# Performance work log

Hardware: AMD Instinct MI355X
Metric: run time of the kernel (lower is better)

Reference implementation:

```python
import jax, jax.numpy as jnp
import numpy as np

L, H, C = 2, 2, 128            # conv layers, heads, out_channels
N, E, B = 10000, 100000, 64    # nodes, edges, graphs
F_NODE, F_EDGE, FC = 92, 50, 512
HC, C3 = H * C, 3 * C


def _ln(x, g, b, eps=1e-5):
    m = x.mean(-1, keepdims=True)
    v = jnp.var(x, axis=-1, keepdims=True)
    return (x - m) * jax.lax.rsqrt(v + eps) * g + b


def setup_inputs() -> dict:
    key = jax.random.key(0)
    ks = jax.random.split(key, 20)
    r = lambda i, shape, s=0.05: jax.random.normal(ks[i], shape, jnp.float32) * s
    d = {}
    d["x"] = jax.random.normal(ks[0], (N, F_NODE), jnp.float32)
    d["edge_attr"] = jax.random.normal(ks[1], (E, F_EDGE), jnp.float32)
    d["pge"] = jax.random.normal(ks[2], (B, 32), jnp.float32)
    d["cse"] = jax.random.normal(ks[3], (B, 7), jnp.float32)
    d["edge_index"] = jax.random.randint(ks[4], (2, E), 0, N, jnp.int32)
    d["batch"] = jnp.sort(jax.random.randint(ks[5], (N,), 0, B, jnp.int32))
    d["atom_W"] = r(6, (F_NODE, C)); d["atom_b"] = jnp.zeros(C)
    d["edge_W"] = r(7, (F_EDGE, C)); d["edge_b"] = jnp.zeros(C)
    d["Wq"] = r(8, (L, C, HC)); d["bq"] = jnp.zeros((L, HC))
    d["Wk"] = r(9, (L, C, HC)); d["bk"] = jnp.zeros((L, HC))
    d["Wv"] = r(10, (L, C, HC)); d["bv"] = jnp.zeros((L, HC))
    d["We"] = r(11, (L, C, HC))
    d["Wmu"] = r(12, (L, C3, C3)); d["bmu"] = jnp.zeros((L, C3))
    d["Wm"] = r(13, (L, C3, C)); d["bm"] = jnp.zeros((L, C))
    d["ln_m_g"] = jnp.ones((L, C)); d["ln_m_b"] = jnp.zeros((L, C))
    d["ln_a_g"] = jnp.ones((L, C3)); d["ln_a_b"] = jnp.zeros((L, C3))
    d["Wc"] = r(14, (L, HC, C)); d["bc"] = jnp.zeros((L, C))
    d["bn_g"] = jnp.ones((L, C)); d["bn_b"] = jnp.zeros((L, C))
    d["Wskip"] = r(15, (L, C, C)); d["bskip"] = jnp.zeros((L, C))
    d["fc_W"] = r(16, (C + 32 + 7, FC)); d["fc_b"] = jnp.zeros(FC)
    d["out_W"] = r(17, (FC, 1)); d["out_b"] = jnp.zeros(1)
    return d


def reference(x, edge_attr, pge, cse, edge_index, batch, atom_W, atom_b,
              edge_W, edge_b, Wq, bq, Wk, bk, Wv, bv, We, Wmu, bmu, Wm, bm,
              ln_m_g, ln_m_b, ln_a_g, ln_a_b, Wc, bc, bn_g, bn_b, Wskip,
              bskip, fc_W, fc_b, out_W, out_b):
    src, dst = edge_index[0], edge_index[1]  # j = source, i = target
    nf = x @ atom_W + atom_b                 # [N, C]
    ef = edge_attr @ edge_W + edge_b         # [E, C]
    scale = 1.0 / np.sqrt(C3).astype(np.float32)
    for i in range(L):
        q = (nf @ Wq[i] + bq[i]).reshape(N, H, C)
        k = (nf @ Wk[i] + bk[i]).reshape(N, H, C)
        v = (nf @ Wv[i] + bv[i]).reshape(N, H, C)
        ea = (ef @ We[i]).reshape(E, H, C)
        qi = q[dst]
        qcat = jnp.concatenate([qi, qi, qi], -1)                 # [E,H,3C]
        kcat = jnp.concatenate([k[dst], k[src], ea], -1)         # [E,H,3C]
        alpha = qcat * kcat * scale
        gate = jax.nn.sigmoid(_ln(alpha, ln_a_g[i], ln_a_b[i]))
        m = jnp.concatenate([v[dst], v[src], ea], -1)            # [E,H,3C]
        m = (jnp.einsum('ehf,fg->ehg', m, Wmu[i]) + bmu[i]) * gate
        m = jnp.einsum('ehf,fc->ehc', m, Wm[i]) + bm[i]          # [E,H,C]
        m = _ln(m, ln_m_g[i], ln_m_b[i])
        agg = jax.ops.segment_sum(m, dst, num_segments=N)        # scatter-add
        o = agg.reshape(N, HC) @ Wc[i] + bc[i]                   # lin_concate
        mu = o.mean(0); var = jnp.var(o, axis=0)                 # BN (batch stats)
        o = (o - mu) * jax.lax.rsqrt(var + 1e-5) * bn_g[i] + bn_b[i]
        o = jax.nn.silu(o)
        nf = o + nf @ Wskip[i] + bskip[i]                        # root skip
    sums = jax.ops.segment_sum(nf, batch, num_segments=B)
    cnt = jax.ops.segment_sum(jnp.ones((N, 1), nf.dtype), batch, num_segments=B)
    pooled = sums / jnp.maximum(cnt, 1.0)                        # global_mean_pool
    feats = jnp.concatenate([pooled, pge, cse], 1)               # [B, C+39]
    h = jax.nn.silu(feats @ fc_W + fc_b)
    return h @ out_W + out_b                                     # [B, 1]
```

## Files before the change

### kernel.cpp

```cpp
#include <hip/hip_runtime.h>
#include <math.h>

#define N_NODES 10000
#define N_EDGES 100000
#define N_GRAPH 64
#define CDIM 128
#define HCDIM 256
#define C3DIM 384

typedef unsigned short u16;
typedef __attribute__((ext_vector_type(8))) short bf16x8;
typedef __attribute__((ext_vector_type(4))) float f32x4;

__device__ __forceinline__ u16 f2bf(float f) {
  union { float f; unsigned int u; } x; x.f = f;
  unsigned int u = x.u + 0x7fffu + ((x.u >> 16) & 1u);
  return (u16)(u >> 16);
}
__device__ __forceinline__ float bf2f(u16 h) {
  union { unsigned int u; float f; } x; x.u = ((unsigned int)h) << 16;
  return x.f;
}

template<int ACT>
__global__ __launch_bounds__(256) void gemm_kernel(
    const float* __restrict__ A, const float* __restrict__ W,
    const float* __restrict__ bias, float* __restrict__ Y,
    u16* __restrict__ Yb, int M, int K, int N) {
  __shared__ float As[16][68];
  __shared__ float Bs[16][65];
  const int tid = threadIdx.x;
  const int bm = blockIdx.y * 64, bn = blockIdx.x * 64;
  const int tx = tid & 15, ty = tid >> 4;
  float acc[4][4] = {};
  for (int k0 = 0; k0 < K; k0 += 16) {
#pragma unroll
    for (int i = 0; i < 4; ++i) {
      int l = tid + i * 256;
      int kk = l & 15, m = l >> 4;
      int gm = bm + m, gk = k0 + kk;
      As[kk][m] = (gm < M && gk < K) ? A[(size_t)gm * K + gk] : 0.f;
    }
#pragma unroll
    for (int i = 0; i < 4; ++i) {
      int l = tid + i * 256;
      int n = l & 63, kk = l >> 6;
      int gk = k0 + kk, gn = bn + n;
      Bs[kk][n] = (gk < K && gn < N) ? W[(size_t)gk * N + gn] : 0.f;
    }
    __syncthreads();
#pragma unroll
    for (int kk = 0; kk < 16; ++kk) {
      float a[4], b[4];
#pragma unroll
      for (int i = 0; i < 4; ++i) a[i] = As[kk][ty * 4 + i];
#pragma unroll
      for (int j = 0; j < 4; ++j) b[j] = Bs[kk][tx * 4 + j];
#pragma unroll
      for (int i = 0; i < 4; ++i)
#pragma unroll
        for (int j = 0; j < 4; ++j) acc[i][j] += a[i] * b[j];
    }
    __syncthreads();
  }
#pragma unroll
  for (int i = 0; i < 4; ++i) {
    int gm = bm + ty * 4 + i;
    if (gm >= M) continue;
#pragma unroll
    for (int j = 0; j < 4; ++j) {
      int gn = bn + tx * 4 + j;
      if (gn >= N) continue;
      float val = acc[i][j] + (bias ? bias[gn] : 0.f);
      if (ACT == 1) val = val / (1.f + expf(-val));
      if (Y)  Y[(size_t)gm * N + gn] = val;
      if (Yb) Yb[(size_t)gm * N + gn] = f2bf(val);
    }
  }
}

template<int OUT_BF16>
__global__ __launch_bounds__(256) void mfma_gemm_kernel(
    const u16* __restrict__ Ab, const u16* __restrict__ WT,
    const float* __restrict__ bias, void* __restrict__ Y,
    int M, int K, int N) {
  const int tid = threadIdx.x;
  const int w = tid >> 6, l = tid & 63;
  const int lq = l >> 4, ln = l & 15;
  const int bm = blockIdx.y * 128, bn = blockIdx.x * 64;
  int ra = bm + w * 32 + ln;      if (ra > M - 1) ra = M - 1;
  int rb = bm + w * 32 + 16 + ln; if (rb > M - 1) rb = M - 1;
  f32x4 acc[2][4];
#pragma unroll
  for (int g = 0; g < 2; ++g)
#pragma unroll
    for (int nt = 0; nt < 4; ++nt) acc[g][nt] = {0.f, 0.f, 0.f, 0.f};
  for (int k0 = 0; k0 < K; k0 += 32) {
    bf16x8 a0 = *(const bf16x8*)&Ab[(size_t)ra * K + k0 + lq * 8];
    bf16x8 a1 = *(const bf16x8*)&Ab[(size_t)rb * K + k0 + lq * 8];
#pragma unroll
    for (int nt = 0; nt < 4; ++nt) {
      bf16x8 b = *(const bf16x8*)&WT[(size_t)(bn + nt * 16 + ln) * K + k0 + lq * 8];
      acc[0][nt] = __builtin_amdgcn_mfma_f32_16x16x32_bf16(a0, b, acc[0][nt], 0, 0, 0);
      acc[1][nt] = __builtin_amdgcn_mfma_f32_16x16x32_bf16(a1, b, acc[1][nt], 0, 0, 0);
    }
  }
#pragma unroll
  for (int g = 0; g < 2; ++g) {
    int rowbase = bm + w * 32 + g * 16 + lq * 4;
#pragma unroll
    for (int nt = 0; nt < 4; ++nt) {
      int gn = bn + nt * 16 + ln;
      float bv = bias ? bias[gn] : 0.f;
#pragma unroll
      for (int r = 0; r < 4; ++r) {
        int gm = rowbase + r;
        if (gm < M) {
          float val = acc[g][nt][r] + bv;
          if (OUT_BF16) ((u16*)Y)[(size_t)gm * N + gn] = f2bf(val);
          else          ((float*)Y)[(size_t)gm * N + gn] = val;
        }
      }
    }
  }
}

__global__ __launch_bounds__(256) void compose_kernel(
    const float* __restrict__ Wv, const float* __restrict__ We,
    const float* __restrict__ Wmu, float* __restrict__ WP12,
    float* __restrict__ WPe) {
  const int z = blockIdx.z;
  const float* Ap; const float* Bp; float* Cp; int ldc;
  if (z < 4) {
    int part = z >> 1, h = z & 1;
    Ap = Wv + h * 128; Bp = Wmu + part * 128 * 384;
    Cp = WP12 + part * 768 + h * 384; ldc = 1536;
  } else {
    int h = z - 4;
    Ap = We + h * 128; Bp = Wmu + 256 * 384;
    Cp = WPe + h * 384; ldc = 768;
  }
  __shared__ float As[16][68];
  __shared__ float Bs[16][65];
  const int tid = threadIdx.x;
  const int bm = blockIdx.y * 64, bn = blockIdx.x * 64;
  const int tx = tid & 15, ty = tid >> 4;
  float acc[4][4] = {};
  for (int k0 = 0; k0 < 128; k0 += 16) {
#pragma unroll
    for (int i = 0; i < 4; ++i) {
      int l = tid + i * 256;
      int kk = l & 15, m = l >> 4;
      As[kk][m] = Ap[(size_t)(bm + m) * 256 + k0 + kk];
    }
#pragma unroll
    for (int i = 0; i < 4; ++i) {
      int l = tid + i * 256;
      int n = l & 63, kk = l >> 6;
      Bs[kk][n] = Bp[(size_t)(k0 + kk) * 384 + bn + n];
    }
    __syncthreads();
#pragma unroll
    for (int kk = 0; kk < 16; ++kk) {
      float a[4], b[4];
#pragma unroll
      for (int i = 0; i < 4; ++i) a[i] = As[kk][ty * 4 + i];
#pragma unroll
      for (int j = 0; j < 4; ++j) b[j] = Bs[kk][tx * 4 + j];
#pragma unroll
      for (int i = 0; i < 4; ++i)
#pragma unroll
        for (int j = 0; j < 4; ++j) acc[i][j] += a[i] * b[j];
    }
    __syncthreads();
  }
#pragma unroll
  for (int i = 0; i < 4; ++i)
#pragma unroll
    for (int j = 0; j < 4; ++j)
      Cp[(size_t)(bm + ty * 4 + i) * ldc + bn + tx * 4 + j] = acc[i][j];
}

__global__ void pack_all_kernel(
    const float* __restrict__ Wq, const float* __restrict__ Wk,
    const float* __restrict__ Wc, const float* __restrict__ Wsk,
    const float* __restrict__ Wm_l, const float* __restrict__ bmu,
    const float* __restrict__ bv_l, const float* __restrict__ Wmu,
    const float* __restrict__ bq_l, const float* __restrict__ bk_l,
    u16* __restrict__ WallT, u16* __restrict__ WcTw, u16* __restrict__ WskT,
    u16* __restrict__ WmTb, float* __restrict__ cbv, float* __restrict__ ball) {
  int z = blockIdx.y;
  int idx = blockIdx.x * 256 + threadIdx.x;
  if (z == 0) {
    if (idx < 32768) { int col = idx >> 7, kk = idx & 127;
      WallT[(size_t)col * 128 + kk] = f2bf(Wq[(size_t)kk * 256 + col]); }
  } else if (z == 1) {
    if (idx < 32768) { int col = idx >> 7, kk = idx & 127;
      WallT[(size_t)(256 + col) * 128 + kk] = f2bf(Wk[(size_t)kk * 256 + col]); }
  } else if (z == 2) {
    if (idx < 32768) { int col = idx >> 8, kk = idx & 255;
      WcTw[(size_t)col * 256 + kk] = f2bf(Wc[(size_t)kk * 128 + col]); }
  } else if (z == 3) {
    if (idx < 16384) { int col = idx >> 7, kk = idx & 127;
      WskT[(size_t)col * 128 + kk] = f2bf(Wsk[(size_t)kk * 128 + col]); }
  } else if (z == 4) {
    if (idx < 49152) { int col = idx / 384, kk = idx - col * 384;
      WmTb[idx] = f2bf(Wm_l[(size_t)kk * 128 + col]); }
  } else if (z == 5) {
    if (idx < 768) {
      int h2 = idx / 384, g = idx - h2 * 384;
      float s = bmu[g];
      for (int d = 0; d < 128; ++d)
        s += bv_l[h2 * 128 + d] * (Wmu[(size_t)d * 384 + g] + Wmu[(size_t)(128 + d) * 384 + g]);
      cbv[idx] = s;
    }
  } else {
    if (idx < 2048) {
      float v = 0.f;
      if (idx < 256) v = bq_l[idx];
      else if (idx < 512) v = bk_l[idx - 256];
      ball[idx] = v;
    }
  }
}

__global__ void packcomb_kernel(const float* __restrict__ We_l,
                                const float* __restrict__ WPe,
                                const float* __restrict__ WP12,
                                u16* __restrict__ WcT, u16* __restrict__ WallT) {
  int z = blockIdx.y;
  int idx = blockIdx.x * 256 + threadIdx.x;
  if (z == 0) {
    if (idx < 131072) { int col = idx >> 7, kk = idx & 127;
      float v = (col < 256) ? We_l[(size_t)kk * 256 + col]
                            : WPe[(size_t)kk * 768 + (col - 256)];
      WcT[idx] = f2bf(v); }
  } else {
    if (idx < 196608) { int col = idx >> 7, kk = idx & 127;
      WallT[(size_t)(512 + col) * 128 + kk] = f2bf(WP12[(size_t)kk * 1536 + col]); }
  }
}

__global__ void pack_bf16_kernel(const float* __restrict__ A, u16* __restrict__ B, int n) {
  int idx = blockIdx.x * blockDim.x + threadIdx.x;
  if (idx < n) B[idx] = f2bf(A[idx]);
}

__global__ __launch_bounds__(256, 3) void edge_kernel(
    const u16* __restrict__ qkp, const u16* __restrict__ efb,
    const int* __restrict__ ei, const u16* __restrict__ WcT,
    const float* __restrict__ cbv,
    const float* __restrict__ lag, const float* __restrict__ lab,
    const u16* __restrict__ WmT, const float* __restrict__ bm_l,
    const float* __restrict__ lmg, const float* __restrict__ lmb,
    float* __restrict__ agg, int E) {
  __shared__ __align__(16) u16 C1[16 * 1032];
  __shared__ __align__(16) u16 A2p[12 * 512];
  __shared__ int did16[16];
  float* C2 = (float*)A2p;
  const int tid = threadIdx.x;
  const int e0 = blockIdx.x * 16;
  const int w = tid >> 6, l = tid & 63;
  const int lq = l >> 4, ln = l & 15;
  const float scale = 0.051031036307982884f;

  if (tid < 16) did16[tid] = ei[E + e0 + tid];

  const int r = tid >> 4, lx = tid & 15;
  const int hA = r >> 3, eA = r & 7;

  bf16x8 qv[2], kdv[2], ksv[2], pdv[2][3], psv[2][3];
#pragma unroll
  for (int s = 0; s < 2; ++s) {
    int edge = e0 + s * 8 + eA;
    int dstn = ei[E + edge], srcn = ei[edge];
    const u16* db = qkp + (size_t)dstn * 2048;
    const u16* sb = qkp + (size_t)srcn * 2048;
    qv[s]  = *(const bf16x8*)&db[hA * 128 + lx * 8];
    kdv[s] = *(const bf16x8*)&db[256 + hA * 128 + lx * 8];
    ksv[s] = *(const bf16x8*)&sb[256 + hA * 128 + lx * 8];
#pragma unroll
    for (int p = 0; p < 3; ++p) {
      pdv[s][p] = *(const bf16x8*)&db[512 + hA * 384 + p * 128 + lx * 8];
      psv[s][p] = *(const bf16x8*)&sb[512 + 768 + hA * 384 + p * 128 + lx * 8];
    }
  }

  {
    bf16x8 afr[4];
    const u16* ab = efb + (size_t)(e0 + ln) * 128 + lq * 8;
#pragma unroll
    for (int ks = 0; ks < 4; ++ks) afr[ks] = *(const bf16x8*)(ab + ks * 32);
    for (int nt = 0; nt < 16; ++nt) {
      int g = w * 16 + nt;
      const u16* bb = WcT + (size_t)(g * 16 + ln) * 128 + lq * 8;
      f32x4 acc = {0.f, 0.f, 0.f, 0.f};
#pragma unroll
      for (int ks = 0; ks < 4; ++ks)
        acc = __builtin_amdgcn_mfma_f32_16x16x32_bf16(
            afr[ks], *(const bf16x8*)(bb + ks * 32), acc, 0, 0, 0);
      int col = g * 16 + ln;
#pragma unroll
      for (int rr = 0; rr < 4; ++rr) C1[(lq * 4 + rr) * 1032 + col] = f2bf(acc[rr]);
    }
  }
  __syncthreads();

  for (int s = 0; s < 2; ++s) {
    {
      bf16x8 sea = *(const bf16x8*)&C1[(s * 8 + eA) * 1032 + hA * 128 + lx * 8];
      float a0[8], a1[8], a2[8];
      float sacc = 0.f, s2acc = 0.f;
#pragma unroll
      for (int j = 0; j < 8; ++j) {
        float qf = bf2f((u16)qv[s][j]);
        float x0 = qf * bf2f((u16)kdv[s][j]) * scale;
        float x1 = qf * bf2f((u16)ksv[s][j]) * scale;
        float x2 = qf * bf2f((u16)sea[j]) * scale;
        a0[j] = x0; a1[j] = x1; a2[j] = x2;
        sacc += x0 + x1 + x2;
        s2acc += x0 * x0 + x1 * x1 + x2 * x2;
      }
#pragma unroll
      for (int mm = 1; mm < 16; mm <<= 1) {
        sacc += __shfl_xor(sacc, mm); s2acc += __shfl_xor(s2acc, mm);
      }
      float mean = sacc * (1.f / C3DIM);
      float rstd = rsqrtf(s2acc * (1.f / C3DIM) - mean * mean + 1e-5f);
#pragma unroll
      for (int p = 0; p < 3; ++p) {
        const float* lg = lag + p * 128 + lx * 8;
        const float* lb = lab + p * 128 + lx * 8;
        f32x4 g0 = *(const f32x4*)lg, g1 = *(const f32x4*)(lg + 4);
        f32x4 b0 = *(const f32x4*)lb, b1 = *(const f32x4*)(lb + 4);
        f32x4 c0 = *(const f32x4*)&cbv[hA * 384 + p * 128 + lx * 8];
        f32x4 c1 = *(const f32x4*)&cbv[hA * 384 + p * 128 + lx * 8 + 4];
        bf16x8 pe = *(const bf16x8*)&C1[(s * 8 + eA) * 1032 + 256 + hA * 384 + p * 128 + lx * 8];
        bf16x8 outv;
#pragma unroll
        for (int j = 0; j < 8; ++j) {
          float av = p == 0 ? a0[j] : (p == 1 ? a1[j] : a2[j]);
          float gg = j < 4 ? g0[j] : g1[j - 4];
          float bb2 = j < 4 ? b0[j] : b1[j - 4];
          float cbj = j < 4 ? c0[j] : c1[j - 4];
          float z = (av - mean) * rstd * gg + bb2;
          float gate = 1.f / (1.f + expf(-z));
          float t = (bf2f((u16)pe[j]) + bf2f((u16)pdv[s][p][j]) +
                     bf2f((u16)psv[s][p][j]) + cbj) * gate;
          outv[j] = (short)f2bf(t);
        }
        int ks = p * 4 + (lx >> 2), qq = lx & 3;
        int slot = (((r ^ (qq << 2)) + ks) & 15) | (qq << 4);
        *(bf16x8*)&A2p[ks * 512 + slot * 8] = outv;
      }
    }
    __syncthreads();

    {
      bf16x8 af2[12];
#pragma unroll
      for (int ks = 0; ks < 12; ++ks) {
        int slot = (((ln ^ (lq << 2)) + ks) & 15) | (lq << 4);
        af2[ks] = *(const bf16x8*)&A2p[ks * 512 + slot * 8];
      }
      __syncthreads();
#pragma unroll
      for (int nt = 0; nt < 2; ++nt) {
        int g = w * 2 + nt;
        const u16* bb = WmT + (size_t)(g * 16 + ln) * 384 + lq * 8;
        f32x4 acc = {0.f, 0.f, 0.f, 0.f};
#pragma unroll
        for (int ks = 0; ks < 12; ++ks)
          acc = __builtin_amdgcn_mfma_f32_16x16x32_bf16(
              af2[ks], *(const bf16x8*)(bb + ks * 32), acc, 0, 0, 0);
        int col = g * 16 + ln;
        float bcol = bm_l[col];
#pragma unroll
        for (int rr = 0; rr < 4; ++rr) C2[(lq * 4 + rr) * 132 + col] = acc[rr] + bcol;
      }
    }
    __syncthreads();

    {
      for (int rw = w; rw < 16; rw += 4) {
        float v0 = C2[rw * 132 + l], v1 = C2[rw * 132 + l + 64];
        float sa = v0 + v1, s2a = v0 * v0 + v1 * v1;
#pragma unroll
        for (int off2 = 32; off2 > 0; off2 >>= 1) {
          sa += __shfl_down(sa, off2); s2a += __shfl_down(s2a, off2);
        }
        sa = __shfl(sa, 0); s2a = __shfl(s2a, 0);
        float mean = sa * (1.f / CDIM);
        float rstd = rsqrtf(s2a * (1.f / CDIM) - mean * mean + 1e-5f);
        int h = rw >> 3, e = rw & 7;
        int dstn = did16[s * 8 + e];
        float o0 = (v0 - mean) * rstd * lmg[l] + lmb[l];
        float o1 = (v1 - mean) * rstd * lmg[l + 64] + lmb[l + 64];
        atomicAdd(&agg[(size_t)dstn * HCDIM + h * CDIM + l], o0);
        atomicAdd(&agg[(size_t)dstn * HCDIM + h * CDIM + l + 64], o1);
      }
    }
    __syncthreads();
  }
}

__global__ __launch_bounds__(256) void bn_stats_kernel(
    const float* __restrict__ o, float* __restrict__ mu, float* __restrict__ rstd) {
  int c = blockIdx.x, tid = threadIdx.x;
  float s = 0.f, s2 = 0.f;
  for (int r = tid; r < N_NODES; r += 256) {
    float x = o[(size_t)r * CDIM + c];
    s += x; s2 += x * x;
  }
  __shared__ float red[8];
#pragma unroll
  for (int off = 32; off > 0; off >>= 1) {
    s += __shfl_down(s, off); s2 += __shfl_down(s2, off);
  }
  if ((tid & 63) == 0) { red[tid >> 6] = s; red[4 + (tid >> 6)] = s2; }
  __syncthreads();
  if (tid == 0) {
    float ts = red[0] + red[1] + red[2] + red[3];
    float t2 = red[4] + red[5] + red[6] + red[7];
    float m = ts * (1.f / N_NODES);
    float var = t2 * (1.f / N_NODES) - m * m;
    mu[c] = m;
    rstd[c] = rsqrtf(var + 1e-5f);
  }
}

__global__ void bn_silu_skip_kernel(
    const float* __restrict__ o, const float* __restrict__ skip,
    const float* __restrict__ mu, const float* __restrict__ rstd,
    const float* __restrict__ g, const float* __restrict__ b,
    float* __restrict__ nf, u16* __restrict__ nfb) {
  int idx = blockIdx.x * blockDim.x + threadIdx.x;
  if (idx >= N_NODES * CDIM) return;
  int c = idx & (CDIM - 1);
  float x = (o[idx] - mu[c]) * rstd[c] * g[c] + b[c];
  float sig = 1.f / (1.f + expf(-x));
  float val = x * sig + skip[idx];
  nf[idx] = val;
  nfb[idx] = f2bf(val);
}

__global__ void pool_kernel(const float* __restrict__ nf, const int* __restrict__ batch,
                            float* __restrict__ psum, float* __restrict__ cnt) {
  int idx = blockIdx.x * blockDim.x + threadIdx.x;
  if (idx >= N_NODES * CDIM) return;
  int n = idx >> 7, c = idx & 127;
  int b = batch[n];
  atomicAdd(&psum[b * CDIM + c], nf[idx]);
  if (c == 0) atomicAdd(&cnt[b], 1.f);
}

__global__ void feats_kernel(const float* __restrict__ psum, const float* __restrict__ cnt,
                             const float* __restrict__ pge, const float* __restrict__ cse,
                             float* __restrict__ feats) {
  int idx = blockIdx.x * blockDim.x + threadIdx.x;
  if (idx >= N_GRAPH * 167) return;
  int b = idx / 167, j = idx - b * 167;
  float val;
  if (j < 128)      val = psum[b * CDIM + j] / fmaxf(cnt[b], 1.f);
  else if (j < 160) val = pge[b * 32 + (j - 128)];
  else              val = cse[b * 7 + (j - 160)];
  feats[idx] = val;
}

__global__ __launch_bounds__(256) void out_kernel(
    const float* __restrict__ h, const float* __restrict__ ow,
    const float* __restrict__ ob, float* __restrict__ out) {
  int b = blockIdx.x, tid = threadIdx.x;
  float s = h[b * 512 + tid] * ow[tid] + h[b * 512 + tid + 256] * ow[tid + 256];
  __shared__ float red[4];
#pragma unroll
  for (int off = 32; off > 0; off >>= 1) s += __shfl_down(s, off);
  if ((tid & 63) == 0) red[tid >> 6] = s;
  __syncthreads();
  if (tid == 0) out[b] = red[0] + red[1] + red[2] + red[3] + ob[0];
}

extern "C" void kernel_launch(void* const* d_in, const int* in_sizes, int n_in,
                              void* d_out, int out_size, void* d_ws, size_t ws_size,
                              hipStream_t stream) {
  const float* x         = (const float*)d_in[0];
  const float* edge_attr = (const float*)d_in[1];
  const float* pge       = (const float*)d_in[2];
  const float* cse       = (const float*)d_in[3];
  const int*   ei        = (const int*)d_in[4];
  const int*   batch     = (const int*)d_in[5];
  const float* atom_W    = (const float*)d_in[6];
  const float* atom_b    = (const float*)d_in[7];
  const float* edge_W    = (const float*)d_in[8];
  const float* edge_b    = (const float*)d_in[9];
  const float* Wq        = (const float*)d_in[10];
  const float* bq        = (const float*)d_in[11];
  const float* Wk        = (const float*)d_in[12];
  const float* bk        = (const float*)d_in[13];
  const float* Wv        = (const float*)d_in[14];
  const float* bv        = (const float*)d_in[15];
  const float* We        = (const float*)d_in[16];
  const float* Wmu       = (const float*)d_in[17];
  const float* bmu       = (const float*)d_in[18];
  const float* Wm        = (const float*)d_in[19];
  const float* bm        = (const float*)d_in[20];
  const float* ln_m_g    = (const float*)d_in[21];
  const float* ln_m_b    = (const float*)d_in[22];
  const float* ln_a_g    = (const float*)d_in[23];
  const float* ln_a_b    = (const float*)d_in[24];
  const float* Wc        = (const float*)d_in[25];
  const float* bc        = (const float*)d_in[26];
  const float* bn_g      = (const float*)d_in[27];
  const float* bn_b      = (const float*)d_in[28];
  const float* Wskip     = (const float*)d_in[29];
  const float* bskip     = (const float*)d_in[30];
  const float* fc_W      = (const float*)d_in[31];
  const float* fc_b      = (const float*)d_in[32];
  const float* out_W     = (const float*)d_in[33];
  const float* out_b     = (const float*)d_in[34];

  float* ws = (float*)d_ws;
  size_t off = 0;
  float* nf    = ws + off; off += (size_t)N_NODES * CDIM;
  float* agg   = ws + off; off += (size_t)N_NODES * HCDIM;
  float* o     = ws + off; off += (size_t)N_NODES * CDIM;
  float* skip  = ws + off; off += (size_t)N_NODES * CDIM;
  float* WP12  = ws + off; off += (size_t)128 * 1536;
  float* WPe   = ws + off; off += (size_t)128 * 768;
  float* cbv   = ws + off; off += 768;
  float* ball  = ws + off; off += 2048;
  float* mu    = ws + off; off += CDIM;
  float* rstd  = ws + off; off += CDIM;
  float* psum  = ws + off; off += (size_t)N_GRAPH * CDIM;
  float* cnt   = ws + off; off += N_GRAPH;
  float* feats = ws + off; off += (size_t)N_GRAPH * 167;
  float* h     = ws + off; off += (size_t)N_GRAPH * 512;
  u16* efb   = (u16*)(ws + off); off += (size_t)N_EDGES * 64;
  u16* WcT   = (u16*)(ws + off); off += 65536;
  u16* WmTb  = (u16*)(ws + off); off += 24576;
  u16* nfb   = (u16*)(ws + off); off += (size_t)N_NODES * 64;
  u16* aggb  = (u16*)(ws + off); off += (size_t)N_NODES * 128;
  u16* qkp   = (u16*)(ws + off); off += (size_t)N_NODES * 1024;
  u16* WallT = (u16*)(ws + off); off += 131072;
  u16* WcTw  = (u16*)(ws + off); off += 16384;
  u16* WskT  = (u16*)(ws + off); off += 8192;

  auto mgemm = [&](const u16* Ab, const u16* WT, const float* bias, void* Y,
                   int M, int K, int Nn, int out_bf16) {
    dim3 grid(Nn / 64, (M + 127) / 128);
    if (out_bf16) mfma_gemm_kernel<1><<<grid, 256, 0, stream>>>(Ab, WT, bias, Y, M, K, Nn);
    else          mfma_gemm_kernel<0><<<grid, 256, 0, stream>>>(Ab, WT, bias, Y, M, K, Nn);
  };

  gemm_kernel<0><<<dim3(2, 157), 256, 0, stream>>>(x, atom_W, atom_b, nf, nfb,
                                                   N_NODES, 92, CDIM);
  gemm_kernel<0><<<dim3(2, 1563), 256, 0, stream>>>(edge_attr, edge_W, edge_b,
                                                    nullptr, efb, N_EDGES, 50, CDIM);

  for (int i = 0; i < 2; ++i) {
    const float* Wv_i  = Wv + (size_t)i * CDIM * HCDIM;
    const float* We_i  = We + (size_t)i * CDIM * HCDIM;
    const float* Wmu_i = Wmu + (size_t)i * C3DIM * C3DIM;
    compose_kernel<<<dim3(6, 2, 6), 256, 0, stream>>>(Wv_i, We_i, Wmu_i, WP12, WPe);
    pack_all_kernel<<<dim3(192, 7), 256, 0, stream>>>(
        Wq + (size_t)i * CDIM * HCDIM, Wk + (size_t)i * CDIM * HCDIM,
        Wc + (size_t)i * HCDIM * CDIM, Wskip + (size_t)i * CDIM * CDIM,
        Wm + (size_t)i * C3DIM * CDIM, bmu + i * C3DIM, bv + i * HCDIM, Wmu_i,
        bq + i * HCDIM, bk + i * HCDIM,
        WallT, WcTw, WskT, WmTb, cbv, ball);
    packcomb_kernel<<<dim3(768, 2), 256, 0, stream>>>(We_i, WPe, WP12, WcT, WallT);

    mgemm(nfb, WallT, ball, qkp, N_NODES, CDIM, 2048, 1);

    hipMemsetAsync(agg, 0, (size_t)N_NODES * HCDIM * sizeof(float), stream);
    edge_kernel<<<dim3(N_EDGES / 16), dim3(256), 0, stream>>>(
        qkp, efb, ei, WcT, cbv,
        ln_a_g + i * C3DIM, ln_a_b + i * C3DIM,
        WmTb, bm + i * CDIM,
        ln_m_g + i * CDIM, ln_m_b + i * CDIM, agg, N_EDGES);

    pack_bf16_kernel<<<dim3((N_NODES * 256 + 255) / 256), dim3(256), 0, stream>>>(
        agg, aggb, N_NODES * 256);
    mgemm(aggb, WcTw, bc + i * CDIM, o, N_NODES, HCDIM, CDIM, 0);
    bn_stats_kernel<<<dim3(CDIM), dim3(256), 0, stream>>>(o, mu, rstd);
    mgemm(nfb, WskT, bskip + i * CDIM, skip, N_NODES, CDIM, CDIM, 0);
    bn_silu_skip_kernel<<<dim3((N_NODES * CDIM + 255) / 256), dim3(256), 0, stream>>>(
        o, skip, mu, rstd, bn_g + i * CDIM, bn_b + i * CDIM, nf, nfb);
  }

  hipMemsetAsync(psum, 0, (size_t)(N_GRAPH * CDIM + N_GRAPH) * sizeof(float), stream);
  pool_kernel<<<dim3((N_NODES * CDIM + 255) / 256), dim3(256), 0, stream>>>(nf, batch, psum, cnt);
  feats_kernel<<<dim3((N_GRAPH * 167 + 255) / 256), dim3(256), 0, stream>>>(psum, cnt, pge, cse, feats);
  gemm_kernel<1><<<dim3(8, 1), 256, 0, stream>>>(feats, fc_W, fc_b, h, nullptr,
                                                 N_GRAPH, 167, 512);
  out_kernel<<<dim3(N_GRAPH), 256, 0, stream>>>(h, out_W, out_b, (float*)d_out);
}
```

Measured before the change: 1.360 ms.

## Sort edges by destination, pre-reduce scatter atomics, fuse BN stats and memsets

Builds a destination-sorted edge permutation with histogram, scan and scatter kernels, so the edge kernel processes edges grouped by target node. Each warp can then accumulate consecutive same-destination contributions in registers before issuing atomics. It also moves the input embeddings to bf16 MFMA GEMMs with padded packing, folds BatchNorm column statistics into the output GEMM via atomics, and folds the agg and pool memsets into existing kernels. This trades extra setup kernels and a permuted gather on edge features for fewer global atomics and launches. The fused statistics compute variance as E[x^2]-m^2 on float atomics, which is less exact than the old two-pass reduction.

```diff
diff --git a/kernel.cpp b/kernel.cpp
--- a/kernel.cpp
+++ b/kernel.cpp
@@ -26,7 +26,7 @@
 __global__ __launch_bounds__(256) void gemm_kernel(
     const float* __restrict__ A, const float* __restrict__ W,
     const float* __restrict__ bias, float* __restrict__ Y,
-    u16* __restrict__ Yb, int M, int K, int N) {
+    int M, int K, int N) {
   __shared__ float As[16][68];
   __shared__ float Bs[16][65];
   const int tid = threadIdx.x;
@@ -73,16 +73,16 @@
       if (gn >= N) continue;
       float val = acc[i][j] + (bias ? bias[gn] : 0.f);
       if (ACT == 1) val = val / (1.f + expf(-val));
-      if (Y)  Y[(size_t)gm * N + gn] = val;
-      if (Yb) Yb[(size_t)gm * N + gn] = f2bf(val);
-    }
-  }
-}
-
-template<int OUT_BF16>
+      Y[(size_t)gm * N + gn] = val;
+    }
+  }
+}
+
+template<int OUT_BF16, int DO_STATS>
 __global__ __launch_bounds__(256) void mfma_gemm_kernel(
     const u16* __restrict__ Ab, const u16* __restrict__ WT,
     const float* __restrict__ bias, void* __restrict__ Y,
+    u16* __restrict__ Ymirror, float* __restrict__ cs, float* __restrict__ cs2,
     int M, int K, int N) {
   const int tid = threadIdx.x;
   const int w = tid >> 6, l = tid & 63;
@@ -119,9 +119,101 @@
           float val = acc[g][nt][r] + bv;
           if (OUT_BF16) ((u16*)Y)[(size_t)gm * N + gn] = f2bf(val);
           else          ((float*)Y)[(size_t)gm * N + gn] = val;
+          if (Ymirror)  Ymirror[(size_t)gm * N + gn] = f2bf(val);
         }
       }
     }
+  }
+  if (DO_STATS) {
+#pragma unroll
+    for (int nt = 0; nt < 4; ++nt) {
+      int gn = bn + nt * 16 + ln;
+      float bv = bias ? bias[gn] : 0.f;
+      float s = 0.f, s2 = 0.f;
+#pragma unroll
+      for (int g = 0; g < 2; ++g) {
+        int rowbase = bm + w * 32 + g * 16 + lq * 4;
+#pragma unroll
+        for (int r = 0; r < 4; ++r) {
+          if (rowbase + r < M) {
+            float v = acc[g][nt][r] + bv;
+            s += v; s2 += v * v;
+          }
+        }
+      }
+      s += __shfl_xor(s, 16); s2 += __shfl_xor(s2, 16);
+      s += __shfl_xor(s, 32); s2 += __shfl_xor(s2, 32);
+      if (lq == 0) { atomicAdd(&cs[gn], s); atomicAdd(&cs2[gn], s2); }
+    }
+  }
+}
+
+__global__ void hist_kernel(const int* __restrict__ ei, int* __restrict__ cnt, int E) {
+  int idx = blockIdx.x * blockDim.x + threadIdx.x;
+  if (idx < E) atomicAdd(&cnt[ei[E + idx]], 1);
+}
+
+__global__ __launch_bounds__(256) void scan_kernel(const int* __restrict__ cnt,
+                                                   int* __restrict__ offs) {
+  __shared__ int wsum[4];
+  __shared__ int carry_s;
+  int tid = threadIdx.x, lane = tid & 63, w = tid >> 6;
+  if (tid == 0) carry_s = 0;
+  __syncthreads();
+  for (int base = 0; base < N_NODES; base += 256) {
+    int v = (base + tid < N_NODES) ? cnt[base + tid] : 0;
+    int incl = v;
+#pragma unroll
+    for (int off = 1; off < 64; off <<= 1) {
+      int t = __shfl_up(incl, off);
+      if (lane >= off) incl += t;
+    }
+    if (lane == 63) wsum[w] = incl;
+    __syncthreads();
+    int woff = 0;
+    for (int i = 0; i < w; ++i) woff += wsum[i];
+    int carry = carry_s;
+    if (base + tid < N_NODES) offs[base + tid] = carry + woff + incl - v;
+    __syncthreads();
+    if (tid == 0) carry_s = carry + wsum[0] + wsum[1] + wsum[2] + wsum[3];
+    __syncthreads();
+  }
+}
+
+__global__ void scatter_kernel(const int* __restrict__ ei, int* __restrict__ offs,
+                               int* __restrict__ perm, int E) {
+  int idx = blockIdx.x * blockDim.x + threadIdx.x;
+  if (idx < E) {
+    int d = ei[E + idx];
+    int pos = atomicAdd(&offs[d], 1);
+    perm[pos] = idx;
+  }
+}
+
+__global__ void pack_init_kernel(
+    const float* __restrict__ x, const float* __restrict__ ea,
+    const float* __restrict__ atom_W, const float* __restrict__ edge_W,
+    u16* __restrict__ xpad, u16* __restrict__ epad,
+    u16* __restrict__ atomWT, u16* __restrict__ WeT2) {
+  int z = blockIdx.y;
+  int idx0 = blockIdx.x * 256 + threadIdx.x;
+  const int stride = 256 * 256;
+  if (z == 0) {
+    for (int idx = idx0; idx < N_NODES * 96; idx += stride) {
+      int n = idx / 96, k = idx - n * 96;
+      xpad[idx] = (k < 92) ? f2bf(x[(size_t)n * 92 + k]) : (u16)0;
+    }
+  } else if (z == 1) {
+    for (int idx = idx0; idx < N_EDGES * 64; idx += stride) {
+      int e = idx >> 6, k = idx & 63;
+      epad[idx] = (k < 50) ? f2bf(ea[(size_t)e * 50 + k]) : (u16)0;
+    }
+  } else if (z == 2) {
+    if (idx0 < 128 * 96) { int n = idx0 / 96, k = idx0 - n * 96;
+      atomWT[idx0] = (k < 92) ? f2bf(atom_W[(size_t)k * 128 + n]) : (u16)0; }
+  } else {
+    if (idx0 < 128 * 64) { int n = idx0 >> 6, k = idx0 & 63;
+      WeT2[idx0] = (k < 50) ? f2bf(edge_W[(size_t)k * 128 + n]) : (u16)0; }
   }
 }
 
@@ -188,7 +280,8 @@
     const float* __restrict__ bv_l, const float* __restrict__ Wmu,
     const float* __restrict__ bq_l, const float* __restrict__ bk_l,
     u16* __restrict__ WallT, u16* __restrict__ WcTw, u16* __restrict__ WskT,
-    u16* __restrict__ WmTb, float* __restrict__ cbv, float* __restrict__ ball) {
+    u16* __restrict__ WmTb, float* __restrict__ cbv, float* __restrict__ ball,
+    float* __restrict__ agg, float* __restrict__ cs, float* __restrict__ cs2) {
   int z = blockIdx.y;
   int idx = blockIdx.x * 256 + threadIdx.x;
   if (z == 0) {
@@ -214,13 +307,16 @@
         s += bv_l[h2 * 128 + d] * (Wmu[(size_t)d * 384 + g] + Wmu[(size_t)(128 + d) * 384 + g]);
       cbv[idx] = s;
     }
-  } else {
+  } else if (z == 6) {
     if (idx < 2048) {
       float v = 0.f;
       if (idx < 256) v = bq_l[idx];
       else if (idx < 512) v = bk_l[idx - 256];
       ball[idx] = v;
     }
+  } else {
+    for (int p = idx; p < N_NODES * HCDIM; p += 192 * 256) agg[p] = 0.f;
+    if (idx < 128) { cs[idx] = 0.f; cs2[idx] = 0.f; }
   }
 }
 
@@ -248,8 +344,8 @@
 
 __global__ __launch_bounds__(256, 3) void edge_kernel(
     const u16* __restrict__ qkp, const u16* __restrict__ efb,
-    const int* __restrict__ ei, const u16* __restrict__ WcT,
-    const float* __restrict__ cbv,
+    const int* __restrict__ ei, const int* __restrict__ perm,
+    const u16* __restrict__ WcT, const float* __restrict__ cbv,
     const float* __restrict__ lag, const float* __restrict__ lab,
     const u16* __restrict__ WmT, const float* __restrict__ bm_l,
     const float* __restrict__ lmg, const float* __restrict__ lmb,
@@ -264,7 +360,7 @@
   const int lq = l >> 4, ln = l & 15;
   const float scale = 0.051031036307982884f;
 
-  if (tid < 16) did16[tid] = ei[E + e0 + tid];
+  if (tid < 16) { int e = perm[e0 + tid]; did16[tid] = ei[E + e]; }
 
   const int r = tid >> 4, lx = tid & 15;
   const int hA = r >> 3, eA = r & 7;
@@ -272,8 +368,8 @@
   bf16x8 qv[2], kdv[2], ksv[2], pdv[2][3], psv[2][3];
 #pragma unroll
   for (int s = 0; s < 2; ++s) {
-    int edge = e0 + s * 8 + eA;
-    int dstn = ei[E + edge], srcn = ei[edge];
+    int e = perm[e0 + s * 8 + eA];
+    int dstn = ei[E + e], srcn = ei[e];
     const u16* db = qkp + (size_t)dstn * 2048;
     const u16* sb = qkp + (size_t)srcn * 2048;
     qv[s]  = *(const bf16x8*)&db[hA * 128 + lx * 8];
@@ -287,8 +383,9 @@
   }
 
   {
+    int er = perm[e0 + ln];
     bf16x8 afr[4];
-    const u16* ab = efb + (size_t)(e0 + ln) * 128 + lq * 8;
+    const u16* ab = efb + (size_t)er * 128 + lq * 8;
 #pragma unroll
     for (int ks = 0; ks < 4; ++ks) afr[ks] = *(const bf16x8*)(ab + ks * 32);
     for (int nt = 0; nt < 16; ++nt) {
@@ -305,6 +402,10 @@
     }
   }
   __syncthreads();
+
+  float agg0 = 0.f, agg1 = 0.f;
+  int cur = -1;
+  const int hW = w >> 1;
 
   for (int s = 0; s < 2; ++s) {
     {
@@ -382,7 +483,10 @@
     __syncthreads();
 
     {
-      for (int rw = w; rw < 16; rw += 4) {
+#pragma unroll
+      for (int i = 0; i < 4; ++i) {
+        int rw = w * 4 + i;
+        int e = rw & 7;
         float v0 = C2[rw * 132 + l], v1 = C2[rw * 132 + l + 64];
         float sa = v0 + v1, s2a = v0 * v0 + v1 * v1;
 #pragma unroll
@@ -392,56 +496,43 @@
         sa = __shfl(sa, 0); s2a = __shfl(s2a, 0);
         float mean = sa * (1.f / CDIM);
         float rstd = rsqrtf(s2a * (1.f / CDIM) - mean * mean + 1e-5f);
-        int h = rw >> 3, e = rw & 7;
-        int dstn = did16[s * 8 + e];
         float o0 = (v0 - mean) * rstd * lmg[l] + lmb[l];
         float o1 = (v1 - mean) * rstd * lmg[l + 64] + lmb[l + 64];
-        atomicAdd(&agg[(size_t)dstn * HCDIM + h * CDIM + l], o0);
-        atomicAdd(&agg[(size_t)dstn * HCDIM + h * CDIM + l + 64], o1);
-      }
-    }
-    __syncthreads();
-  }
-}
-
-__global__ __launch_bounds__(256) void bn_stats_kernel(
-    const float* __restrict__ o, float* __restrict__ mu, float* __restrict__ rstd) {
-  int c = blockIdx.x, tid = threadIdx.x;
-  float s = 0.f, s2 = 0.f;
-  for (int r = tid; r < N_NODES; r += 256) {
-    float x = o[(size_t)r * CDIM + c];
-    s += x; s2 += x * x;
-  }
-  __shared__ float red[8];
-#pragma unroll
-  for (int off = 32; off > 0; off >>= 1) {
-    s += __shfl_down(s, off); s2 += __shfl_down(s2, off);
-  }
-  if ((tid & 63) == 0) { red[tid >> 6] = s; red[4 + (tid >> 6)] = s2; }
-  __syncthreads();
-  if (tid == 0) {
-    float ts = red[0] + red[1] + red[2] + red[3];
-    float t2 = red[4] + red[5] + red[6] + red[7];
-    float m = ts * (1.f / N_NODES);
-    float var = t2 * (1.f / N_NODES) - m * m;
-    mu[c] = m;
-    rstd[c] = rsqrtf(var + 1e-5f);
+        int dstn = did16[s * 8 + e];
+        if (dstn != cur) {
+          if (cur >= 0) {
+            atomicAdd(&agg[(size_t)cur * HCDIM + hW * CDIM + l], agg0);
+            atomicAdd(&agg[(size_t)cur * HCDIM + hW * CDIM + l + 64], agg1);
+          }
+          cur = dstn; agg0 = o0; agg1 = o1;
+        } else { agg0 += o0; agg1 += o1; }
+      }
+    }
+    __syncthreads();
+  }
+  if (cur >= 0) {
+    atomicAdd(&agg[(size_t)cur * HCDIM + hW * CDIM + l], agg0);
+    atomicAdd(&agg[(size_t)cur * HCDIM + hW * CDIM + l + 64], agg1);
   }
 }
 
 __global__ void bn_silu_skip_kernel(
     const float* __restrict__ o, const float* __restrict__ skip,
-    const float* __restrict__ mu, const float* __restrict__ rstd,
+    const float* __restrict__ cs, const float* __restrict__ cs2,
     const float* __restrict__ g, const float* __restrict__ b,
-    float* __restrict__ nf, u16* __restrict__ nfb) {
+    float* __restrict__ nf, u16* __restrict__ nfb, float* __restrict__ pz) {
   int idx = blockIdx.x * blockDim.x + threadIdx.x;
   if (idx >= N_NODES * CDIM) return;
   int c = idx & (CDIM - 1);
-  float x = (o[idx] - mu[c]) * rstd[c] * g[c] + b[c];
+  float m = cs[c] * (1.f / N_NODES);
+  float var = cs2[c] * (1.f / N_NODES) - m * m;
+  float rstd = rsqrtf(var + 1e-5f);
+  float x = (o[idx] - m) * rstd * g[c] + b[c];
   float sig = 1.f / (1.f + expf(-x));
   float val = x * sig + skip[idx];
   nf[idx] = val;
   nfb[idx] = f2bf(val);
+  if (pz && idx < N_GRAPH * CDIM + N_GRAPH) pz[idx] = 0.f;
 }
 
 __global__ void pool_kernel(const float* __restrict__ nf, const int* __restrict__ batch,
@@ -529,12 +620,15 @@
   float* WPe   = ws + off; off += (size_t)128 * 768;
   float* cbv   = ws + off; off += 768;
   float* ball  = ws + off; off += 2048;
-  float* mu    = ws + off; off += CDIM;
-  float* rstd  = ws + off; off += CDIM;
+  float* csum  = ws + off; off += CDIM;
+  float* csum2 = ws + off; off += CDIM;
   float* psum  = ws + off; off += (size_t)N_GRAPH * CDIM;
   float* cnt   = ws + off; off += N_GRAPH;
   float* feats = ws + off; off += (size_t)N_GRAPH * 167;
   float* h     = ws + off; off += (size_t)N_GRAPH * 512;
+  int* scnt    = (int*)(ws + off); off += N_NODES;
+  int* soffs   = (int*)(ws + off); off += N_NODES;
+  int* perm    = (int*)(ws + off); off += N_EDGES;
   u16* efb   = (u16*)(ws + off); off += (size_t)N_EDGES * 64;
   u16* WcT   = (u16*)(ws + off); off += 65536;
   u16* WmTb  = (u16*)(ws + off); off += 24576;
@@ -544,54 +638,57 @@
   u16* WallT = (u16*)(ws + off); off += 131072;
   u16* WcTw  = (u16*)(ws + off); off += 16384;
   u16* WskT  = (u16*)(ws + off); off += 8192;
-
-  auto mgemm = [&](const u16* Ab, const u16* WT, const float* bias, void* Y,
-                   int M, int K, int Nn, int out_bf16) {
-    dim3 grid(Nn / 64, (M + 127) / 128);
-    if (out_bf16) mfma_gemm_kernel<1><<<grid, 256, 0, stream>>>(Ab, WT, bias, Y, M, K, Nn);
-    else          mfma_gemm_kernel<0><<<grid, 256, 0, stream>>>(Ab, WT, bias, Y, M, K, Nn);
-  };
-
-  gemm_kernel<0><<<dim3(2, 157), 256, 0, stream>>>(x, atom_W, atom_b, nf, nfb,
-                                                   N_NODES, 92, CDIM);
-  gemm_kernel<0><<<dim3(2, 1563), 256, 0, stream>>>(edge_attr, edge_W, edge_b,
-                                                    nullptr, efb, N_EDGES, 50, CDIM);
+  u16* xpad  = (u16*)(ws + off); off += (size_t)N_NODES * 48;
+  u16* epad  = (u16*)(ws + off); off += (size_t)N_EDGES * 32;
+  u16* atomWT= (u16*)(ws + off); off += 6144;
+  u16* WeT2  = (u16*)(ws + off); off += 4096;
+
+  hipMemsetAsync(scnt, 0, N_NODES * sizeof(int), stream);
+  hist_kernel<<<dim3((N_EDGES + 255) / 256), 256, 0, stream>>>(ei, scnt, N_EDGES);
+  scan_kernel<<<dim3(1), 256, 0, stream>>>(scnt, soffs);
+  scatter_kernel<<<dim3((N_EDGES + 255) / 256), 256, 0, stream>>>(ei, soffs, perm, N_EDGES);
+  pack_init_kernel<<<dim3(256, 4), 256, 0, stream>>>(x, edge_attr, atom_W, edge_W,
+                                                     xpad, epad, atomWT, WeT2);
+  mfma_gemm_kernel<0, 0><<<dim3(2, 79), 256, 0, stream>>>(
+      xpad, atomWT, atom_b, nf, nfb, nullptr, nullptr, N_NODES, 96, CDIM);
+  mfma_gemm_kernel<1, 0><<<dim3(2, 782), 256, 0, stream>>>(
+      epad, WeT2, edge_b, efb, nullptr, nullptr, nullptr, N_EDGES, 64, CDIM);
 
   for (int i = 0; i < 2; ++i) {
     const float* Wv_i  = Wv + (size_t)i * CDIM * HCDIM;
     const float* We_i  = We + (size_t)i * CDIM * HCDIM;
     const float* Wmu_i = Wmu + (size_t)i * C3DIM * C3DIM;
     compose_kernel<<<dim3(6, 2, 6), 256, 0, stream>>>(Wv_i, We_i, Wmu_i, WP12, WPe);
-    pack_all_kernel<<<dim3(192, 7), 256, 0, stream>>>(
+    pack_all_kernel<<<dim3(192, 8), 256, 0, stream>>>(
         Wq + (size_t)i * CDIM * HCDIM, Wk + (size_t)i * CDIM * HCDIM,
         Wc + (size_t)i * HCDIM * CDIM, Wskip + (size_t)i * CDIM * CDIM,
         Wm + (size_t)i * C3DIM * CDIM, bmu + i * C3DIM, bv + i * HCDIM, Wmu_i,
         bq + i * HCDIM, bk + i * HCDIM,
-        WallT, WcTw, WskT, WmTb, cbv, ball);
+        WallT, WcTw, WskT, WmTb, cbv, ball, agg, csum, csum2);
     packcomb_kernel<<<dim3(768, 2), 256, 0, stream>>>(We_i, WPe, WP12, WcT, WallT);
 
-    mgemm(nfb, WallT, ball, qkp, N_NODES, CDIM, 2048, 1);
-
-    hipMemsetAsync(agg, 0, (size_t)N_NODES * HCDIM * sizeof(float), stream);
+    mfma_gemm_kernel<1, 0><<<dim3(32, 79), 256, 0, stream>>>(
+        nfb, WallT, ball, qkp, nullptr, nullptr, nullptr, N_NODES, CDIM, 2048);
+
     edge_kernel<<<dim3(N_EDGES / 16), dim3(256), 0, stream>>>(
-        qkp, efb, ei, WcT, cbv,
+        qkp, efb, ei, perm, WcT, cbv,
         ln_a_g + i * C3DIM, ln_a_b + i * C3DIM,
         WmTb, bm + i * CDIM,
         ln_m_g + i * CDIM, ln_m_b + i * CDIM, agg, N_EDGES);
 
     pack_bf16_kernel<<<dim3((N_NODES * 256 + 255) / 256), dim3(256), 0, stream>>>(
         agg, aggb, N_NODES * 256);
-    mgemm(aggb, WcTw, bc + i * CDIM, o, N_NODES, HCDIM, CDIM, 0);
-    bn_stats_kernel<<<dim3(CDIM), dim3(256), 0, stream>>>(o, mu, rstd);
-    mgemm(nfb, WskT, bskip + i * CDIM, skip, N_NODES, CDIM, CDIM, 0);
+    mfma_gemm_kernel<0, 1><<<dim3(2, 79), 256, 0, stream>>>(
+        aggb, WcTw, bc + i * CDIM, o, nullptr, csum, csum2, N_NODES, HCDIM, CDIM);
+    mfma_gemm_kernel<0, 0><<<dim3(2, 79), 256, 0, stream>>>(
+        nfb, WskT, bskip + i * CDIM, skip, nullptr, nullptr, nullptr, N_NODES, CDIM, CDIM);
     bn_silu_skip_kernel<<<dim3((N_NODES * CDIM + 255) / 256), dim3(256), 0, stream>>>(
-        o, skip, mu, rstd, bn_g + i * CDIM, bn_b + i * CDIM, nf, nfb);
-  }
-
-  hipMemsetAsync(psum, 0, (size_t)(N_GRAPH * CDIM + N_GRAPH) * sizeof(float), stream);
+        o, skip, csum, csum2, bn_g + i * CDIM, bn_b + i * CDIM, nf, nfb,
+        (i == 1) ? psum : nullptr);
+  }
+
   pool_kernel<<<dim3((N_NODES * CDIM + 255) / 256), dim3(256), 0, stream>>>(nf, batch, psum, cnt);
   feats_kernel<<<dim3((N_GRAPH * 167 + 255) / 256), dim3(256), 0, stream>>>(psum, cnt, pge, cse, feats);
-  gemm_kernel<1><<<dim3(8, 1), 256, 0, stream>>>(feats, fc_W, fc_b, h, nullptr,
-                                                 N_GRAPH, 167, 512);
+  gemm_kernel<1><<<dim3(8, 1), 256, 0, stream>>>(feats, fc_W, fc_b, h, N_GRAPH, 167, 512);
   out_kernel<<<dim3(N_GRAPH), 256, 0, stream>>>(h, out_W, out_b, (float*)d_out);
 }
```

Result: slower. 1.922 ms (+41.3%).
